# Kernel optimization log

Measured on AMD Instinct MI355X. Metric: run time of the kernel, lower is better.

Reference implementation:

```python
import jax, jax.numpy as jnp
import numpy as np

B, C, DIM = 8, 2048, 512
H = 512  # hidden_dim
NEG_SLOPE = 0.01  # torch LeakyReLU default


def setup_inputs() -> dict:
    key = jax.random.key(0)
    ks = jax.random.split(key, 8)
    features = jax.random.normal(ks[0], (B, C, DIM), dtype=jnp.float32)
    mask = jax.random.uniform(ks[1], (B, C, C), dtype=jnp.float32)
    s = 0.02
    W_w = jax.random.normal(ks[2], (DIM, 3 * H), dtype=jnp.float32) * s
    b_w = jax.random.normal(ks[3], (3 * H,), dtype=jnp.float32) * s
    a_score = jax.random.normal(ks[4], (2 * H,), dtype=jnp.float32) * s
    b_score = jax.random.normal(ks[5], (1,), dtype=jnp.float32) * s
    W_out = jax.random.normal(ks[6], (H, DIM), dtype=jnp.float32) * s
    b_out = jax.random.normal(ks[7], (DIM,), dtype=jnp.float32) * s
    return {"features": features, "mask": mask, "W_w": W_w, "b_w": b_w,
            "a_score": a_score, "b_score": b_score, "W_out": W_out, "b_out": b_out}


def reference(features, mask, W_w, b_w, a_score, b_score, W_out, b_out):
    # qkv projection: [B,C,3H]
    qkv = features @ W_w + b_w
    q, k, v = jnp.split(qkv, 3, axis=-1)  # each [B,C,H]
    # score(cat([q_i, k_j])) = q_i . a[:H] + k_j . a[H:] + b  (Linear(2H,1))
    sq = q @ a_score[:H]            # [B,C]
    sk = k @ a_score[H:]            # [B,C]
    scores = jax.nn.leaky_relu(sq[:, :, None] + sk[:, None, :] + b_score[0],
                               negative_slope=NEG_SLOPE)  # [B,C,C]
    attn = jax.nn.softmax(scores * mask, axis=-1)           # [B,C,C]
    weighted = jnp.einsum('bij,bjh->bih', attn, v)          # [B,C,H]
    return weighted @ W_out + b_out                          # [B,C,DIM]
```

## Files before the change

kernel.cpp:

```cpp
#include <hip/hip_runtime.h>
#include <hip/hip_bf16.h>

#define B_ 8
#define C_ 2048
#define DIM_ 512
#define NEG_SLOPE 0.01f

typedef short bf16x8 __attribute__((ext_vector_type(8)));
typedef short bf16x4 __attribute__((ext_vector_type(4)));
typedef float f32x4 __attribute__((ext_vector_type(4)));

#define WT_OFF   0
#define UT_OFF   524288
#define FP_OFF   (524288 + 16777216)
#define BCOMB_F  0
#define WQ_F     512
#define WK_F     1024
#define CQB_F    1536
#define CK_F     1537
#define SQP_F    2048
#define SKP_F    18432

static __device__ __forceinline__ unsigned short bf16u(float x) {
    union { __hip_bfloat16 h; unsigned short u; } c;
    c.h = __float2bfloat16(x);
    return c.u;
}

__global__ __launch_bounds__(256) void k_prep(const float* __restrict__ W_w,
                                              const float* __restrict__ W_out,
                                              const float* __restrict__ b_w,
                                              const float* __restrict__ a_score,
                                              const float* __restrict__ b_score,
                                              char* wsb, float* wsf) {
    __shared__ float As[32][34];
    __shared__ float Bs[32][34];
    __shared__ float s1[256], s2[256];
    const int t = threadIdx.x;
    const int bid = blockIdx.x;

    if (bid == 0) {
        s1[t] = b_w[t] * a_score[t] + b_w[t + 256] * a_score[t + 256];
        s2[t] = b_w[512 + t] * a_score[512 + t] + b_w[768 + t] * a_score[768 + t];
        __syncthreads();
        for (int off = 128; off > 0; off >>= 1) {
            if (t < off) { s1[t] += s1[t + off]; s2[t] += s2[t + off]; }
            __syncthreads();
        }
        if (t == 0) { wsf[CQB_F] = s1[0] + b_score[0]; wsf[CK_F] = s2[0]; }
        __syncthreads();
    }

    if (bid >= 128) {
        int wave = t >> 6, lane = t & 63;
        int e = (bid - 128) * 4 + wave;
        const float4* R4 = (const float4*)(W_w + (size_t)e * 1536);
        const float4* A4 = (const float4*)a_score;
        float aq = 0.f, ak = 0.f;
#pragma unroll
        for (int k = 0; k < 2; ++k) {
            float4 f = R4[lane + 64 * k];
            float4 a = A4[lane + 64 * k];
            aq += f.x * a.x + f.y * a.y + f.z * a.z + f.w * a.w;
            float4 g = R4[128 + lane + 64 * k];
            float4 a2 = A4[128 + lane + 64 * k];
            ak += g.x * a2.x + g.y * a2.y + g.z * a2.z + g.w * a2.w;
        }
#pragma unroll
        for (int off = 32; off; off >>= 1) { aq += __shfl_xor(aq, off); ak += __shfl_xor(ak, off); }
        if (lane == 0) { wsf[WQ_F + e] = aq; wsf[WK_F + e] = ak; }
    }

    const int d0 = (bid & 15) * 32;
    const int e0 = (bid >> 4) * 32;
    const int ty = t >> 4, tx = t & 15;
    const int hl = t >> 5, c = t & 31;
    float a00 = 0.f, a01 = 0.f, a10 = 0.f, a11 = 0.f;
    float bc = 0.f;
    for (int k0 = 0; k0 < 512; k0 += 32) {
#pragma unroll
        for (int r = 0; r < 4; ++r) {
            int h = hl + 8 * r;
            As[h][c] = W_out[(size_t)(k0 + h) * 512 + d0 + c];
            Bs[c][h] = W_w[(size_t)(e0 + h) * 1536 + 1024 + k0 + c];
        }
        __syncthreads();
        if (e0 == 0 && t < 32) {
#pragma unroll
            for (int kk = 0; kk < 32; ++kk)
                bc = fmaf(b_w[1024 + k0 + kk], As[kk][t], bc);
        }
#pragma unroll
        for (int kk = 0; kk < 32; ++kk) {
            float2 a2 = *(const float2*)&As[kk][ty * 2];
            float2 b2 = *(const float2*)&Bs[kk][tx * 2];
            a00 = fmaf(a2.x, b2.x, a00);
            a01 = fmaf(a2.x, b2.y, a01);
            a10 = fmaf(a2.y, b2.x, a10);
            a11 = fmaf(a2.y, b2.y, a11);
        }
        __syncthreads();
    }
    unsigned short* Wt = (unsigned short*)(wsb + WT_OFF);
    const int d = d0 + ty * 2, e = e0 + tx * 2;
    Wt[(size_t)d * 512 + e]           = bf16u(a00);
    Wt[(size_t)d * 512 + e + 1]       = bf16u(a01);
    Wt[(size_t)(d + 1) * 512 + e]     = bf16u(a10);
    Wt[(size_t)(d + 1) * 512 + e + 1] = bf16u(a11);
    if (e0 == 0 && t < 32) wsf[BCOMB_F + d0 + t] = bc;
}

__global__ __launch_bounds__(256) void k_ut(const float* __restrict__ F,
                                            char* __restrict__ wsb, float* __restrict__ wsf) {
    __shared__ unsigned short Fb[32][520];
    const int t = threadIdx.x;
    const int bid = blockIdx.x;
    const int b = bid & 7, j0 = (bid >> 3) * 32;
    const unsigned short* Wt = (const unsigned short*)(wsb + WT_OFF);
    unsigned short* Ut = (unsigned short*)(wsb + UT_OFF) + (size_t)b * 512 * 2048;
    const float* Ft = F + ((size_t)(b * C_ + j0)) * 512;

    {
        const int r = t >> 3, g = t & 7;
        const float4* Fr = (const float4*)(F + ((size_t)(b * C_ + j0 + r)) * 512);
        const float4* WQ4 = (const float4*)(wsf + WQ_F);
        const float4* WK4 = (const float4*)(wsf + WK_F);
        float aq = 0.f, ak = 0.f;
#pragma unroll
        for (int cc = 0; cc < 16; ++cc) {
            float4 f = Fr[cc * 8 + g];
            float4 q = WQ4[cc * 8 + g];
            float4 kk = WK4[cc * 8 + g];
            aq += f.x * q.x + f.y * q.y + f.z * q.z + f.w * q.w;
            ak += f.x * kk.x + f.y * kk.y + f.z * kk.z + f.w * kk.w;
        }
        aq += __shfl_xor(aq, 1); aq += __shfl_xor(aq, 2); aq += __shfl_xor(aq, 4);
        ak += __shfl_xor(ak, 1); ak += __shfl_xor(ak, 2); ak += __shfl_xor(ak, 4);
        if (g == 0) {
            wsf[SQP_F + b * C_ + j0 + r] = aq + wsf[CQB_F];
            wsf[SKP_F + b * C_ + j0 + r] = ak + wsf[CK_F];
        }
    }

#pragma unroll
    for (int q = 0; q < 16; ++q) {
        float4 v = *(const float4*)(Ft + (size_t)q * 1024 + t * 4);
        int jr = 2 * q + (t >> 7);
        int e = (t & 127) * 4;
        unsigned int lo = (unsigned int)bf16u(v.x) | ((unsigned int)bf16u(v.y) << 16);
        unsigned int hi = (unsigned int)bf16u(v.z) | ((unsigned int)bf16u(v.w) << 16);
        *(uint2*)&Fb[jr][e] = make_uint2(lo, hi);
    }
    __syncthreads();
    const int l = t & 63, lr = l & 15, lg = l >> 4;
    const int d0 = (t >> 6) * 128;
    f32x4 acc[8][2];
#pragma unroll
    for (int m = 0; m < 8; ++m)
#pragma unroll
        for (int n = 0; n < 2; ++n) acc[m][n] = (f32x4){0.f, 0.f, 0.f, 0.f};
#pragma unroll
    for (int ks = 0; ks < 16; ++ks) {
        bf16x8 af[8], bv[2];
#pragma unroll
        for (int m = 0; m < 8; ++m)
            af[m] = *(const bf16x8*)(Wt + (size_t)(d0 + 16 * m + lr) * 512 + ks * 32 + 8 * lg);
#pragma unroll
        for (int n = 0; n < 2; ++n)
            bv[n] = *(const bf16x8*)&Fb[16 * n + lr][ks * 32 + 8 * lg];
#pragma unroll
        for (int m = 0; m < 8; ++m)
#pragma unroll
            for (int n = 0; n < 2; ++n)
                acc[m][n] = __builtin_amdgcn_mfma_f32_16x16x32_bf16(af[m], bv[n], acc[m][n], 0, 0, 0);
    }
#pragma unroll
    for (int m = 0; m < 8; ++m)
#pragma unroll
        for (int n = 0; n < 2; ++n)
#pragma unroll
            for (int r = 0; r < 4; ++r) {
                int d = d0 + 16 * m + lg * 4 + r;
                int j = j0 + 16 * n + lr;
                Ut[(size_t)d * 2048 + j] = bf16u(acc[m][n][r]);
            }
}


#define BAR \
    asm volatile("s_waitcnt lgkmcnt(0)"); \
    __builtin_amdgcn_s_barrier();

#define MISSUE(M, KT) { \
    const float* mp = mrow + (size_t)(KT) * 128; \
    M##a = __builtin_nontemporal_load((const f32x4*)mp); \
    M##b = __builtin_nontemporal_load((const f32x4*)(mp + 4)); }

#define PCX(KV, MV, I) { \
    float z = sqv + (KV); z = fmaxf(z, z * NEG_SLOPE) * (MV); \
    z = __expf(z); psum += z; vv[I] = (short)bf16u(z); }

#define PCOMP(M, KT) { \
    const int kt = (KT); \
    float4 ka = *(const float4*)&sk_lds[kt * 128 + pjc * 8]; \
    float4 kb = *(const float4*)&sk_lds[kt * 128 + pjc * 8 + 4]; \
    bf16x8 vv; \
    PCX(ka.x, M##a[0], 0) PCX(ka.y, M##a[1], 1) PCX(ka.z, M##a[2], 2) PCX(ka.w, M##a[3], 3) \
    PCX(kb.x, M##b[0], 4) PCX(kb.y, M##b[1], 5) PCX(kb.z, M##b[2], 6) PCX(kb.w, M##b[3], 7) \
    *(bf16x8*)(Pbyte + (kt & 1) * 16384 + prow * 256 + ((pjc ^ (prow & 7)) << 4)) = vv; }

#define LDUT(U, KT) { \
    const int kt = (KT); \
    _Pragma("unroll") \
    for (int n = 0; n < 2; ++n) \
        _Pragma("unroll") \
        for (int ks = 0; ks < 4; ++ks) \
            U[n * 4 + ks] = *(const bf16x8*)(Utw + (size_t)(16 * n + lr) * 2048 \
                                             + kt * 128 + ks * 32 + 8 * lg); }

#define MFMAP(U, KP) { \
    const char* pb = Pbyte + ((KP) & 1) * 16384; \
    _Pragma("unroll") \
    for (int g = 0; g < 4; ++g) { \
        const char* rp = pb + (16 * g + lr) * 256; \
        _Pragma("unroll") \
        for (int ks = 0; ks < 4; ++ks) { \
            bf16x8 a = *(const bf16x8*)(rp + (((ks * 4 + lg) ^ (lr & 7)) << 4)); \
            acc[g][0] = __builtin_amdgcn_mfma_f32_16x16x32_bf16(a, U[ks],     acc[g][0], 0, 0, 0); \
            acc[g][1] = __builtin_amdgcn_mfma_f32_16x16x32_bf16(a, U[4 + ks], acc[g][1], 0, 0, 0); \
        } \
    } }

#define PHASE(M, KP) { \
    const int kp = (KP); \
    LDUT(u, kp) \
    if (kp + 1 < 16) PCOMP(M, kp + 1) \
    if (kp + 3 < 16) MISSUE(M, kp + 3) \
    MFMAP(u, kp) \
    BAR }

__global__ __launch_bounds__(1024, 1) void k_attn(const float* __restrict__ mask,
                                                  const float* __restrict__ b_out,
                                                  char* __restrict__ wsb,
                                                  float* __restrict__ out) {
    __shared__ unsigned short Pt[2][64][128];
    __shared__ float sk_lds[2048];
    __shared__ float bcbo[512];
    __shared__ float psums[64][16];
    __shared__ float rinvs[64];
    const int t = threadIdx.x;
    const int bid = blockIdx.x;
    const int b = bid & 7, i0 = (bid >> 3) * 64;
    const int w = t >> 6, l = t & 63, lr = l & 15, lg = l >> 4;
    const int prow = t >> 4, pjc = t & 15;
    const float* wsf = (const float*)(wsb + FP_OFF);
    const unsigned short* Utw = (const unsigned short*)(wsb + UT_OFF)
                                + (size_t)b * 512 * 2048 + (size_t)(w * 32) * 2048;
    char* Pbyte = (char*)Pt;
    const float sqv = wsf[SQP_F + b * C_ + i0 + prow];
    const float* mrow = mask + ((size_t)(b * C_ + i0 + prow)) * C_ + pjc * 8;

    if (t < 512) {
        const float* skp = wsf + SKP_F + b * C_;
        *(float4*)&sk_lds[t * 4] = *(const float4*)(skp + t * 4);
        bcbo[t & 511] = wsf[BCOMB_F + (t & 511)] + b_out[t & 511];
    }
    __syncthreads();

    f32x4 m0a, m0b, m1a, m1b;
    bf16x8 u[8];
    float psum = 0.f;
    f32x4 acc[4][2];
#pragma unroll
    for (int g = 0; g < 4; ++g)
#pragma unroll
        for (int n = 0; n < 2; ++n) acc[g][n] = (f32x4){0.f, 0.f, 0.f, 0.f};

    MISSUE(m0, 0) MISSUE(m1, 1)
    PCOMP(m0, 0)
    MISSUE(m0, 2)
    BAR

    for (int o = 0; o < 8; ++o) {
        PHASE(m1, 2 * o)
        PHASE(m0, 2 * o + 1)
    }

    psums[prow][pjc] = psum;
    __syncthreads();
    if (t < 64) {
        float s = 0.f;
#pragma unroll
        for (int q = 0; q < 4; ++q) {
            float4 p4 = *(const float4*)&psums[t][q * 4];
            s += p4.x + p4.y + p4.z + p4.w;
        }
        rinvs[t] = 1.0f / s;
    }
    __syncthreads();
#pragma unroll
    for (int g = 0; g < 4; ++g) {
#pragma unroll
        for (int r = 0; r < 4; ++r) {
            const int irow = 16 * g + lg * 4 + r;
            const float rv = rinvs[irow];
            float* orow = out + ((size_t)(b * C_ + i0 + irow)) * DIM_ + w * 32;
#pragma unroll
            for (int n = 0; n < 2; ++n)
                orow[16 * n + lr] = acc[g][n][r] * rv + bcbo[w * 32 + 16 * n + lr];
        }
    }
}

extern "C" void kernel_launch(void* const* d_in, const int* in_sizes, int n_in,
                              void* d_out, int out_size, void* d_ws, size_t ws_size,
                              hipStream_t stream) {
    const float* features = (const float*)d_in[0];
    const float* mask     = (const float*)d_in[1];
    const float* W_w      = (const float*)d_in[2];
    const float* b_w      = (const float*)d_in[3];
    const float* a_score  = (const float*)d_in[4];
    const float* b_score  = (const float*)d_in[5];
    const float* W_out    = (const float*)d_in[6];
    const float* b_out    = (const float*)d_in[7];
    float* out = (float*)d_out;
    char* wsb  = (char*)d_ws;
    float* wsf = (float*)(wsb + FP_OFF);

    k_prep<<<256, 256, 0, stream>>>(W_w, W_out, b_w, a_score, b_score, wsb, wsf);
    k_ut<<<512, 256, 0, stream>>>(features, wsb, wsf);
    k_attn<<<256, 1024, 0, stream>>>(mask, b_out, wsb, out);
}
```

Before: 152.9 us.

## Warp-specialize attention kernel into producer P-compute and consumer MFMA waves

Splits the 16 waves into 8 producer waves that stream the mask and compute exp-scores into LDS, and 8 consumer waves that load U^T and run the MFMAs. The K tile shrinks from 128 to 64 over 32 phases, and the mask prefetch depth grows to three buffers. Consumer waves raise their scheduling priority around the MFMAs, and sched_barriers pin the barrier ordering. The goal is to overlap memory-bound mask streaming with matrix work. In exchange it adds more barriers per unit of work and leaves fewer waves on each role.

```diff
diff --git a/kernel.cpp b/kernel.cpp
--- a/kernel.cpp
+++ b/kernel.cpp
@@ -7,7 +7,6 @@
 #define NEG_SLOPE 0.01f
 
 typedef short bf16x8 __attribute__((ext_vector_type(8)));
-typedef short bf16x4 __attribute__((ext_vector_type(4)));
 typedef float f32x4 __attribute__((ext_vector_type(4)));
 
 #define WT_OFF   0
@@ -188,11 +187,14 @@
 
 
 #define BAR \
+    __builtin_amdgcn_sched_barrier(0); \
     asm volatile("s_waitcnt lgkmcnt(0)"); \
-    __builtin_amdgcn_s_barrier();
+    __builtin_amdgcn_sched_barrier(0); \
+    __builtin_amdgcn_s_barrier(); \
+    __builtin_amdgcn_sched_barrier(0);
 
 #define MISSUE(M, KT) { \
-    const float* mp = mrow + (size_t)(KT) * 128; \
+    const float* mp = mrow + (size_t)(KT) * 64; \
     M##a = __builtin_nontemporal_load((const f32x4*)mp); \
     M##b = __builtin_nontemporal_load((const f32x4*)(mp + 4)); }
 
@@ -202,63 +204,34 @@
 
 #define PCOMP(M, KT) { \
     const int kt = (KT); \
-    float4 ka = *(const float4*)&sk_lds[kt * 128 + pjc * 8]; \
-    float4 kb = *(const float4*)&sk_lds[kt * 128 + pjc * 8 + 4]; \
+    float4 ka = *(const float4*)&sk_lds[kt * 64 + pjc * 8]; \
+    float4 kb = *(const float4*)&sk_lds[kt * 64 + pjc * 8 + 4]; \
     bf16x8 vv; \
     PCX(ka.x, M##a[0], 0) PCX(ka.y, M##a[1], 1) PCX(ka.z, M##a[2], 2) PCX(ka.w, M##a[3], 3) \
     PCX(kb.x, M##b[0], 4) PCX(kb.y, M##b[1], 5) PCX(kb.z, M##b[2], 6) PCX(kb.w, M##b[3], 7) \
-    *(bf16x8*)(Pbyte + (kt & 1) * 16384 + prow * 256 + ((pjc ^ (prow & 7)) << 4)) = vv; }
-
-#define LDUT(U, KT) { \
-    const int kt = (KT); \
-    _Pragma("unroll") \
-    for (int n = 0; n < 2; ++n) \
-        _Pragma("unroll") \
-        for (int ks = 0; ks < 4; ++ks) \
-            U[n * 4 + ks] = *(const bf16x8*)(Utw + (size_t)(16 * n + lr) * 2048 \
-                                             + kt * 128 + ks * 32 + 8 * lg); }
-
-#define MFMAP(U, KP) { \
-    const char* pb = Pbyte + ((KP) & 1) * 16384; \
-    _Pragma("unroll") \
-    for (int g = 0; g < 4; ++g) { \
-        const char* rp = pb + (16 * g + lr) * 256; \
-        _Pragma("unroll") \
-        for (int ks = 0; ks < 4; ++ks) { \
-            bf16x8 a = *(const bf16x8*)(rp + (((ks * 4 + lg) ^ (lr & 7)) << 4)); \
-            acc[g][0] = __builtin_amdgcn_mfma_f32_16x16x32_bf16(a, U[ks],     acc[g][0], 0, 0, 0); \
-            acc[g][1] = __builtin_amdgcn_mfma_f32_16x16x32_bf16(a, U[4 + ks], acc[g][1], 0, 0, 0); \
-        } \
-    } }
-
-#define PHASE(M, KP) { \
+    *(bf16x8*)(Pbyte + (kt & 1) * 8192 + prow * 128 + ((pjc ^ (prow & 7)) << 4)) = vv; }
+
+#define PPHASE(M, KP) { \
     const int kp = (KP); \
-    LDUT(u, kp) \
-    if (kp + 1 < 16) PCOMP(M, kp + 1) \
-    if (kp + 3 < 16) MISSUE(M, kp + 3) \
-    MFMAP(u, kp) \
+    if (kp + 1 < 32) PCOMP(M, kp + 1) \
+    if (kp + 4 < 32) MISSUE(M, kp + 4) \
     BAR }
 
 __global__ __launch_bounds__(1024, 1) void k_attn(const float* __restrict__ mask,
                                                   const float* __restrict__ b_out,
                                                   char* __restrict__ wsb,
                                                   float* __restrict__ out) {
-    __shared__ unsigned short Pt[2][64][128];
+    __shared__ unsigned short Pt[2][64][64];
     __shared__ float sk_lds[2048];
     __shared__ float bcbo[512];
-    __shared__ float psums[64][16];
+    __shared__ float psums[64][8];
     __shared__ float rinvs[64];
     const int t = threadIdx.x;
     const int bid = blockIdx.x;
     const int b = bid & 7, i0 = (bid >> 3) * 64;
-    const int w = t >> 6, l = t & 63, lr = l & 15, lg = l >> 4;
-    const int prow = t >> 4, pjc = t & 15;
+    const int w = t >> 6;
     const float* wsf = (const float*)(wsb + FP_OFF);
-    const unsigned short* Utw = (const unsigned short*)(wsb + UT_OFF)
-                                + (size_t)b * 512 * 2048 + (size_t)(w * 32) * 2048;
     char* Pbyte = (char*)Pt;
-    const float sqv = wsf[SQP_F + b * C_ + i0 + prow];
-    const float* mrow = mask + ((size_t)(b * C_ + i0 + prow)) * C_ + pjc * 8;
 
     if (t < 512) {
         const float* skp = wsf + SKP_F + b * C_;
@@ -267,49 +240,87 @@
     }
     __syncthreads();
 
-    f32x4 m0a, m0b, m1a, m1b;
-    bf16x8 u[8];
-    float psum = 0.f;
-    f32x4 acc[4][2];
-#pragma unroll
-    for (int g = 0; g < 4; ++g)
-#pragma unroll
-        for (int n = 0; n < 2; ++n) acc[g][n] = (f32x4){0.f, 0.f, 0.f, 0.f};
-
-    MISSUE(m0, 0) MISSUE(m1, 1)
-    PCOMP(m0, 0)
-    MISSUE(m0, 2)
-    BAR
-
-    for (int o = 0; o < 8; ++o) {
-        PHASE(m1, 2 * o)
-        PHASE(m0, 2 * o + 1)
-    }
-
-    psums[prow][pjc] = psum;
+    if (w >= 8) {
+        const int q = t & 511;
+        const int prow = q >> 3, pjc = q & 7;
+        const float sqv = wsf[SQP_F + b * C_ + i0 + prow];
+        const float* mrow = mask + ((size_t)(b * C_ + i0 + prow)) * C_ + pjc * 8;
+        float psum = 0.f;
+        f32x4 m0a, m0b, m1a, m1b, m2a, m2b;
+        MISSUE(m0, 0) MISSUE(m1, 1) MISSUE(m2, 2)
+        PCOMP(m0, 0)
+        MISSUE(m0, 3)
+        BAR
+        for (int o = 0; o < 10; ++o) {
+            PPHASE(m1, 3 * o)
+            PPHASE(m2, 3 * o + 1)
+            PPHASE(m0, 3 * o + 2)
+        }
+        PPHASE(m1, 30)
+        PPHASE(m2, 31)
+        psums[prow][pjc] = psum;
+    } else {
+        const int l = t & 63, lr = l & 15, lg = l >> 4;
+        const int dw = w * 64;
+        const unsigned short* Utw = (const unsigned short*)(wsb + UT_OFF)
+                                    + (size_t)b * 512 * 2048 + (size_t)dw * 2048;
+        f32x4 acc[4][4];
+#pragma unroll
+        for (int g = 0; g < 4; ++g)
+#pragma unroll
+            for (int n = 0; n < 4; ++n) acc[g][n] = (f32x4){0.f, 0.f, 0.f, 0.f};
+        BAR
+        for (int kp = 0; kp < 32; ++kp) {
+            bf16x8 u[8];
+#pragma unroll
+            for (int n = 0; n < 4; ++n) {
+                const unsigned short* up = Utw + (size_t)(16 * n + lr) * 2048 + kp * 64 + 8 * lg;
+                u[2 * n]     = *(const bf16x8*)up;
+                u[2 * n + 1] = *(const bf16x8*)(up + 32);
+            }
+            const char* pb = Pbyte + (kp & 1) * 8192;
+            __builtin_amdgcn_s_setprio(1);
+#pragma unroll
+            for (int g = 0; g < 4; ++g) {
+                const char* rp = pb + (16 * g + lr) * 128;
+                bf16x8 a0 = *(const bf16x8*)(rp + ((lg ^ (lr & 7)) << 4));
+                bf16x8 a1 = *(const bf16x8*)(rp + (((4 + lg) ^ (lr & 7)) << 4));
+#pragma unroll
+                for (int n = 0; n < 4; ++n) {
+                    acc[g][n] = __builtin_amdgcn_mfma_f32_16x16x32_bf16(a0, u[2 * n],     acc[g][n], 0, 0, 0);
+                    acc[g][n] = __builtin_amdgcn_mfma_f32_16x16x32_bf16(a1, u[2 * n + 1], acc[g][n], 0, 0, 0);
+                }
+            }
+            __builtin_amdgcn_s_setprio(0);
+            BAR
+        }
+        __syncthreads();
+        if (t < 64) {
+            float s = 0.f;
+#pragma unroll
+            for (int qq = 0; qq < 2; ++qq) {
+                float4 p4 = *(const float4*)&psums[t][qq * 4];
+                s += p4.x + p4.y + p4.z + p4.w;
+            }
+            rinvs[t] = 1.0f / s;
+        }
+        __syncthreads();
+#pragma unroll
+        for (int g = 0; g < 4; ++g) {
+#pragma unroll
+            for (int r = 0; r < 4; ++r) {
+                const int irow = 16 * g + lg * 4 + r;
+                const float rv = rinvs[irow];
+                float* orow = out + ((size_t)(b * C_ + i0 + irow)) * DIM_ + dw;
+#pragma unroll
+                for (int n = 0; n < 4; ++n)
+                    orow[16 * n + lr] = acc[g][n][r] * rv + bcbo[dw + 16 * n + lr];
+            }
+        }
+        return;
+    }
     __syncthreads();
-    if (t < 64) {
-        float s = 0.f;
-#pragma unroll
-        for (int q = 0; q < 4; ++q) {
-            float4 p4 = *(const float4*)&psums[t][q * 4];
-            s += p4.x + p4.y + p4.z + p4.w;
-        }
-        rinvs[t] = 1.0f / s;
-    }
     __syncthreads();
-#pragma unroll
-    for (int g = 0; g < 4; ++g) {
-#pragma unroll
-        for (int r = 0; r < 4; ++r) {
-            const int irow = 16 * g + lg * 4 + r;
-            const float rv = rinvs[irow];
-            float* orow = out + ((size_t)(b * C_ + i0 + irow)) * DIM_ + w * 32;
-#pragma unroll
-            for (int n = 0; n < 2; ++n)
-                orow[16 * n + lr] = acc[g][n][r] * rv + bcbo[w * 32 + 16 * n + lr];
-        }
-    }
 }
 
 extern "C" void kernel_launch(void* const* d_in, const int* in_sizes, int n_in,
```

Result: faster. 149.3 us (-2.3%).
